# Performance work log

Hardware: AMD Instinct MI355X
Metric: run time of the kernel (lower is better)

The kernel has to match this reference:

```python
import jax, jax.numpy as jnp
import numpy as np

DIM_Q = 1024
DIM_KV = 768
N_HEADS = 4


def setup_inputs() -> dict:
    key = jax.random.key(0)
    ks = jax.random.split(key, 7)
    b, lq, lkv = 4, 2048, 2048
    q = jax.random.normal(ks[0], (b, lq, DIM_Q), dtype=jnp.float32)
    kv = jax.random.normal(ks[1], (b, lkv, DIM_KV), dtype=jnp.float32)
    s_q = 1.0 / np.sqrt(DIM_Q)
    s_kv = 1.0 / np.sqrt(DIM_KV)
    Wq = jax.random.normal(ks[2], (DIM_Q, DIM_Q), dtype=jnp.float32) * s_q
    Wk = jax.random.normal(ks[3], (DIM_Q, DIM_KV), dtype=jnp.float32) * s_kv
    Wv = jax.random.normal(ks[4], (DIM_Q, DIM_KV), dtype=jnp.float32) * s_kv
    Wo = jax.random.normal(ks[5], (DIM_Q, DIM_Q), dtype=jnp.float32) * s_q
    bo = jax.random.normal(ks[6], (DIM_Q,), dtype=jnp.float32) * 0.01
    return {"q": q, "kv": kv, "Wq": Wq, "Wk": Wk, "Wv": Wv, "Wo": Wo, "bo": bo}


def _split_heads(x):
    # [b, l, d] -> [b, h, l, d/h]
    b, l, d = x.shape
    return x.reshape(b, l, N_HEADS, d // N_HEADS).transpose(0, 2, 1, 3)


def reference(q, kv, Wq, Wk, Wv, Wo, bo):
    qp = q @ Wq.T               # [b, lq, dim_q]
    kp = kv @ Wk.T              # [b, lkv, dim_q]
    vp = kv @ Wv.T              # [b, lkv, dim_q]
    qh, kh, vh = _split_heads(qp), _split_heads(kp), _split_heads(vp)
    scale = (DIM_Q // N_HEADS) ** (-0.5)
    scores = jnp.einsum('bhqd,bhkd->bhqk', qh, kh) * scale
    attn = jax.nn.softmax(scores, axis=-1)
    ctx = jnp.einsum('bhqk,bhkd->bhqd', attn, vh)  # [b, h, lq, hd]
    b, h, lq, hd = ctx.shape
    ctx = ctx.transpose(0, 2, 1, 3).reshape(b, lq, h * hd)
    return ctx @ Wo.T + bo
```

## Files before the change

### kernel.cpp

```cpp
#include <hip/hip_runtime.h>

#define DIMQ 1024
#define NH 4
#define HD 256
#define BSZ 4
#define LQ 2048
#define LKV 2048
#define KVN 2048

typedef __attribute__((ext_vector_type(8))) short bf16x8;
typedef __attribute__((ext_vector_type(4))) float f32x4;

__device__ inline unsigned short f32_to_bf16(float f) {
  union { float f; unsigned u; } v; v.f = f;
  unsigned u = v.u;
  return (unsigned short)((u + 0x7fffu + ((u >> 16) & 1u)) >> 16);
}

__device__ inline uint4 ld8cvt(const float* p, float scale) {
  const float4 a = *(const float4*)p;
  const float4 b = *(const float4*)(p + 4);
  union { unsigned short s[8]; uint4 v; } r;
  r.s[0] = f32_to_bf16(a.x * scale); r.s[1] = f32_to_bf16(a.y * scale);
  r.s[2] = f32_to_bf16(a.z * scale); r.s[3] = f32_to_bf16(a.w * scale);
  r.s[4] = f32_to_bf16(b.x * scale); r.s[5] = f32_to_bf16(b.y * scale);
  r.s[6] = f32_to_bf16(b.z * scale); r.s[7] = f32_to_bf16(b.w * scale);
  return r.v;
}

__device__ __forceinline__ void gl2lds16(const void* gptr, void* lptr) {
  __builtin_amdgcn_global_load_lds(
      (const __attribute__((address_space(1))) void*)gptr,
      (__attribute__((address_space(3))) void*)lptr, 16, 0, 0);
}

__global__ __launch_bounds__(256)
void cvt6(const float* s0, const float* s1, const float* s2, const float* s3,
          const float* s4, const float* s5,
          unsigned short* d0, unsigned short* d1, unsigned short* d2,
          unsigned short* d3, unsigned short* d4, unsigned short* d5,
          long n0, long n1, long n2, long n3, long n4, long n5,
          float c0, float c1, float c2, float c3, float c4, float c5) {
  const float* s; unsigned short* d; long n; float c;
  switch (blockIdx.y) {
    case 0: s = s0; d = d0; n = n0; c = c0; break;
    case 1: s = s1; d = d1; n = n1; c = c1; break;
    case 2: s = s2; d = d2; n = n2; c = c2; break;
    case 3: s = s3; d = d3; n = n3; c = c3; break;
    case 4: s = s4; d = d4; n = n4; c = c4; break;
    default: s = s5; d = d5; n = n5; c = c5; break;
  }
  long i = ((long)blockIdx.x * 256 + threadIdx.x) * 8;
  if (i < n) *(uint4*)(d + i) = ld8cvt(s + i, c);
}

__global__ __launch_bounds__(256)
void transpose_k(const unsigned short* __restrict__ vp,
                 unsigned short* __restrict__ vpT,
                 int src_stride, int src_off) {
  __shared__ unsigned short T[64][64];
  const int l0g = blockIdx.x * 64;
  const int b = l0g / LKV, l0 = l0g % LKV;
  const int n0 = blockIdx.y * 64;
  const int tid = threadIdx.x;
  const int r = tid >> 3, c = tid & 7;
#pragma unroll
  for (int p = 0; p < 2; ++p) {
    int row = p * 32 + r;
    *(uint4*)&T[row][(c ^ ((row >> 3) & 7)) * 8] =
        *(const uint4*)(vp + (size_t)(l0g + row) * src_stride + src_off + n0 + c * 8);
  }
  __syncthreads();
#pragma unroll
  for (int p = 0; p < 2; ++p) {
    int n = p * 32 + r;
    union { unsigned short s[8]; uint4 v; } t;
#pragma unroll
    for (int j = 0; j < 8; ++j) {
      int row = c * 8 + j;
      t.s[j] = T[row][(((n >> 3) ^ ((row >> 3) & 7)) << 3) | (n & 7)];
    }
    *(uint4*)(vpT + ((size_t)b * DIMQ + n0 + n) * LKV + l0 + c * 8) = t.v;
  }
}

template<typename TOUT, bool HAS_BIAS>
__global__ __launch_bounds__(256)
void gemm_bt(const unsigned short* __restrict__ A,
             const unsigned short* __restrict__ Bm,
             const float* __restrict__ bias,
             TOUT* __restrict__ C,
             int M, int N, int K) {
  __shared__ alignas(16) unsigned short As[128 * 64];
  __shared__ alignas(16) unsigned short Bs[128 * 64];
  const int tid = threadIdx.x;
  const int lane = tid & 63;
  const int wave = tid >> 6;
  const int wr = (wave >> 1) * 64, wc = (wave & 1) * 64;
  const int l15 = lane & 15, quad = lane >> 4;
  const int srow = lane >> 3, scol = lane & 7;
  const int m0 = blockIdx.x * 128;
  const int n0 = blockIdx.y * 128;

  f32x4 acc[4][4] = {};
  for (int k0 = 0; k0 < K; k0 += 64) {
    __syncthreads();
#pragma unroll
    for (int i = 0; i < 4; ++i) {
      int c = wave * 4 + i;
      gl2lds16(A + (size_t)(m0 + c * 8 + srow) * K + k0 + scol * 8, As + c * 512);
      gl2lds16(Bm + (size_t)(n0 + c * 8 + srow) * K + k0 + scol * 8, Bs + c * 512);
    }
    __syncthreads();
#pragma unroll
    for (int kh = 0; kh < 2; ++kh) {
      bf16x8 af[4], bfr[4];
#pragma unroll
      for (int i = 0; i < 4; ++i)
        af[i] = *(const bf16x8*)(As + (wr + i * 16 + l15) * 64 + kh * 32 + quad * 8);
#pragma unroll
      for (int j = 0; j < 4; ++j)
        bfr[j] = *(const bf16x8*)(Bs + (wc + j * 16 + l15) * 64 + kh * 32 + quad * 8);
#pragma unroll
      for (int i = 0; i < 4; ++i)
#pragma unroll
        for (int j = 0; j < 4; ++j)
          acc[i][j] = __builtin_amdgcn_mfma_f32_16x16x32_bf16(af[i], bfr[j], acc[i][j], 0, 0, 0);
    }
  }

#pragma unroll
  for (int j = 0; j < 4; ++j) {
    int n = n0 + wc + j * 16 + l15;
    float bv = 0.f;
    if (HAS_BIAS) bv = bias[n];
#pragma unroll
    for (int i = 0; i < 4; ++i) {
      int mb = m0 + wr + i * 16 + quad * 4;
#pragma unroll
      for (int r = 0; r < 4; ++r) {
        float v = acc[i][j][r] + bv;
        if constexpr (sizeof(TOUT) == 2)
          C[(size_t)(mb + r) * N + n] = f32_to_bf16(v);
        else
          C[(size_t)(mb + r) * N + n] = v;
      }
    }
  }
}

__global__ __launch_bounds__(256, 2)
void attn(const unsigned short* __restrict__ qp,
          const unsigned short* __restrict__ kpv,
          const unsigned short* __restrict__ vpT,
          unsigned short* __restrict__ ctx) {
  __shared__ alignas(16) unsigned short Ks[64 * 256];
  __shared__ alignas(16) unsigned short Vt[256 * 64];
  __shared__ alignas(16) unsigned short Ps[64 * 64];
  __shared__ float Ls[64][2];
  const int tid = threadIdx.x, lane = tid & 63, wave = tid >> 6;
  const int l15 = lane & 15, quad = lane >> 4;
  const int qh = wave >> 1;
  const int kvh = wave & 1;
  const int lin = blockIdx.x;
  const int work = ((lin & 7) << 6) + (lin >> 3);
  const int b = work >> 7, h = (work >> 5) & 3;
  const int q0 = (work & 31) * 64;
  const size_t base = (size_t)b * LQ * DIMQ + h * HD;

  bf16x8 qf[2][8];
#pragma unroll
  for (int im = 0; im < 2; ++im) {
    const unsigned short* qrow =
        qp + base + (size_t)(q0 + qh * 32 + im * 16 + l15) * DIMQ;
#pragma unroll
    for (int s = 0; s < 8; ++s)
      qf[im][s] = *(const bf16x8*)(qrow + s * 32 + quad * 8);
  }

  f32x4 oacc[4][4] = {};
  float lrow[2][4] = {};

  const unsigned short* kb = kpv + (size_t)b * LKV * KVN + h * HD;
  const unsigned short* vtb = vpT + ((size_t)b * DIMQ + h * HD) * LKV;

  const int krow_l = lane >> 5;
  const int kcol_l = lane & 31;
  const int vrow_l = lane >> 3;
  const int vcol_l = lane & 7;

#pragma unroll
  for (int i = 0; i < 8; ++i) {
    int c = i * 4 + wave;
    int row = 2 * c + krow_l;
    int lr = (row & 32) + ((row & 15) << 1) + ((row >> 4) & 1);
    gl2lds16(kb + (size_t)lr * KVN + ((kcol_l ^ (row & 7)) << 3), Ks + c * 512);
  }
  __syncthreads();

  for (int kv0 = 0; kv0 < LKV; kv0 += 64) {
#pragma unroll
    for (int i = 0; i < 8; ++i) {
      int c = i * 4 + wave;
      int row = 8 * c + vrow_l;
      gl2lds16(vtb + (size_t)row * LKV + kv0 + ((vcol_l ^ (row & 7)) << 3),
               Vt + c * 512);
    }

    f32x4 sacc[2][2] = {};
    const int r0 = kvh * 32 + l15, r1 = r0 + 16;
    __builtin_amdgcn_s_setprio(1);
#pragma unroll
    for (int s = 0; s < 8; ++s) {
      bf16x8 kf0 = *(const bf16x8*)(Ks + r0 * 256 + (((s * 4 + quad) ^ (r0 & 7)) << 3));
      bf16x8 kf1 = *(const bf16x8*)(Ks + r1 * 256 + (((s * 4 + quad) ^ (r1 & 7)) << 3));
      sacc[0][0] = __builtin_amdgcn_mfma_f32_16x16x32_bf16(qf[0][s], kf0, sacc[0][0], 0, 0, 0);
      sacc[0][1] = __builtin_amdgcn_mfma_f32_16x16x32_bf16(qf[0][s], kf1, sacc[0][1], 0, 0, 0);
      sacc[1][0] = __builtin_amdgcn_mfma_f32_16x16x32_bf16(qf[1][s], kf0, sacc[1][0], 0, 0, 0);
      sacc[1][1] = __builtin_amdgcn_mfma_f32_16x16x32_bf16(qf[1][s], kf1, sacc[1][1], 0, 0, 0);
    }
    __builtin_amdgcn_s_setprio(0);

    const int dw = kvh * 16 + l15;
    const int t16 = dw >> 2, sub = dw & 3;
#pragma unroll
    for (int im = 0; im < 2; ++im)
#pragma unroll
      for (int i = 0; i < 4; ++i) {
        int row = qh * 32 + im * 16 + quad * 4 + i;
        float p0 = exp2f(sacc[im][0][i]);
        float p1 = exp2f(sacc[im][1][i]);
        unsigned pw = (unsigned)f32_to_bf16(p0) | ((unsigned)f32_to_bf16(p1) << 16);
        *(unsigned*)(Ps + row * 64 + (((t16 ^ (row & 7)) << 3) | (sub * 2))) = pw;
        lrow[im][i] += p0 + p1;
      }
    __syncthreads();

    if (kv0 + 64 < LKV) {
#pragma unroll
      for (int i = 0; i < 8; ++i) {
        int c = i * 4 + wave;
        int row = 2 * c + krow_l;
        int lr = (row & 32) + ((row & 15) << 1) + ((row >> 4) & 1);
        gl2lds16(kb + (size_t)(kv0 + 64 + lr) * KVN + ((kcol_l ^ (row & 7)) << 3),
                 Ks + c * 512);
      }
    }

    __builtin_amdgcn_s_setprio(1);
#pragma unroll
    for (int u = 0; u < 2; ++u) {
      bf16x8 pf[4], vf[4];
#pragma unroll
      for (int mt = 0; mt < 4; ++mt) {
        int pr = mt * 16 + l15;
        pf[mt] = *(const bf16x8*)(Ps + pr * 64 + (((u * 4 + quad) ^ (pr & 7)) << 3));
      }
#pragma unroll
      for (int nt = 0; nt < 4; ++nt) {
        int vr = wave * 64 + nt * 16 + l15;
        vf[nt] = *(const bf16x8*)(Vt + vr * 64 + (((u * 4 + quad) ^ (vr & 7)) << 3));
      }
#pragma unroll
      for (int mt = 0; mt < 4; ++mt)
#pragma unroll
        for (int nt = 0; nt < 4; ++nt)
          oacc[mt][nt] = __builtin_amdgcn_mfma_f32_16x16x32_bf16(pf[mt], vf[nt], oacc[mt][nt], 0, 0, 0);
    }
    __builtin_amdgcn_s_setprio(0);
    __syncthreads();
  }

#pragma unroll
  for (int im = 0; im < 2; ++im)
#pragma unroll
    for (int i = 0; i < 4; ++i) {
      float l = lrow[im][i];
      l += __shfl_xor(l, 1);
      l += __shfl_xor(l, 2);
      l += __shfl_xor(l, 4);
      l += __shfl_xor(l, 8);
      if (l15 == 0) Ls[qh * 32 + im * 16 + quad * 4 + i][kvh] = l;
    }
  __syncthreads();

  unsigned short* cb = ctx + base;
#pragma unroll
  for (int mt = 0; mt < 4; ++mt)
#pragma unroll
    for (int r = 0; r < 4; ++r) {
      int row = mt * 16 + quad * 4 + r;
      float inv = 1.0f / (Ls[row][0] + Ls[row][1]);
#pragma unroll
      for (int nt = 0; nt < 4; ++nt) {
        int col = wave * 64 + nt * 16 + l15;
        cb[(size_t)(q0 + row) * DIMQ + col] = f32_to_bf16(oacc[mt][nt][r] * inv);
      }
    }
}

extern "C" void kernel_launch(void* const* d_in, const int* in_sizes, int n_in,
                              void* d_out, int out_size, void* d_ws, size_t ws_size,
                              hipStream_t stream) {
  const float* q  = (const float*)d_in[0];
  const float* kv = (const float*)d_in[1];
  const float* Wq = (const float*)d_in[2];
  const float* Wk = (const float*)d_in[3];
  const float* Wv = (const float*)d_in[4];
  const float* Wo = (const float*)d_in[5];
  const float* bo = (const float*)d_in[6];
  float* out = (float*)d_out;

  const long NQ = (long)BSZ * LQ * DIMQ;
  const long NKV = (long)BSZ * LKV * 768;
  const long NWQ = (long)DIMQ * DIMQ;
  const long NWK = (long)DIMQ * 768;

  unsigned short* q_bf = (unsigned short*)d_out;
  unsigned short* kpv  = (unsigned short*)d_out;
  unsigned short* kv_bf = (unsigned short*)d_ws;
  unsigned short* ctx   = kv_bf;
  unsigned short* Wq_bf = kv_bf + NQ;
  unsigned short* Wk_bf = Wq_bf + NWQ;
  unsigned short* Wv_bf = Wk_bf + NWK;
  unsigned short* Wo_bf = Wv_bf + NWK;
  unsigned short* qp    = Wo_bf + NWQ;
  unsigned short* vpT   = qp + NQ;

  dim3 blk(256);
  const int M = BSZ * LQ;

  cvt6<<<dim3(4096, 6), blk, 0, stream>>>(
      kv, Wq, Wk, Wv, Wo, q,
      kv_bf, Wq_bf, Wk_bf, Wv_bf, Wo_bf, q_bf,
      NKV, NWQ, NWK, NWK, NWQ, NQ,
      1.0f, 0.0625f * 1.44269504088896f, 1.0f, 1.0f, 1.0f, 1.0f);
  gemm_bt<unsigned short, false><<<dim3(M/128, DIMQ/128), blk, 0, stream>>>(q_bf, Wq_bf, nullptr, qp, M, DIMQ, 1024);
  gemm_bt<unsigned short, false><<<dim3(M/128, KVN/128), blk, 0, stream>>>(kv_bf, Wk_bf, nullptr, kpv, M, KVN, 768);
  transpose_k<<<dim3(M/64, DIMQ/64), blk, 0, stream>>>(kpv, vpT, KVN, 1024);
  attn<<<dim3(512), blk, 0, stream>>>(qp, kpv, vpT, ctx);
  gemm_bt<float, true><<<dim3(M/128, DIMQ/128), blk, 0, stream>>>(ctx, Wo_bf, bo, out, M, DIMQ, 1024);
}
```

Before: 302.5 us.

## Double-buffer K/V tiles and use 512-thread blocks over 128 query rows

```diff
diff --git a/kernel.cpp b/kernel.cpp
--- a/kernel.cpp
+++ b/kernel.cpp
@@ -149,30 +149,32 @@
   }
 }
 
-__global__ __launch_bounds__(256, 2)
+__global__ __launch_bounds__(512, 1)
 void attn(const unsigned short* __restrict__ qp,
           const unsigned short* __restrict__ kpv,
           const unsigned short* __restrict__ vpT,
           unsigned short* __restrict__ ctx) {
-  __shared__ alignas(16) unsigned short Ks[64 * 256];
-  __shared__ alignas(16) unsigned short Vt[256 * 64];
-  __shared__ alignas(16) unsigned short Ps[64 * 64];
-  __shared__ float Ls[64][2];
+  __shared__ alignas(16) unsigned short Ks[2][64 * 256];
+  __shared__ alignas(16) unsigned short Vt[2][256 * 64];
+  __shared__ alignas(16) unsigned short Ps[128 * 64];
+  __shared__ float Ls[128][2];
   const int tid = threadIdx.x, lane = tid & 63, wave = tid >> 6;
   const int l15 = lane & 15, quad = lane >> 4;
-  const int qh = wave >> 1;
+  const int qqh = wave >> 1;
   const int kvh = wave & 1;
+  const int qh2 = wave >> 2;
+  const int dq  = wave & 3;
   const int lin = blockIdx.x;
-  const int work = ((lin & 7) << 6) + (lin >> 3);
-  const int b = work >> 7, h = (work >> 5) & 3;
-  const int q0 = (work & 31) * 64;
+  const int work = ((lin & 7) << 5) + (lin >> 3);
+  const int b = work >> 6, h = (work >> 4) & 3;
+  const int q0 = (work & 15) * 128;
   const size_t base = (size_t)b * LQ * DIMQ + h * HD;
 
   bf16x8 qf[2][8];
 #pragma unroll
   for (int im = 0; im < 2; ++im) {
     const unsigned short* qrow =
-        qp + base + (size_t)(q0 + qh * 32 + im * 16 + l15) * DIMQ;
+        qp + base + (size_t)(q0 + qqh * 32 + im * 16 + l15) * DIMQ;
 #pragma unroll
     for (int s = 0; s < 8; ++s)
       qf[im][s] = *(const bf16x8*)(qrow + s * 32 + quad * 8);
@@ -189,22 +191,38 @@
   const int vrow_l = lane >> 3;
   const int vcol_l = lane & 7;
 
-#pragma unroll
-  for (int i = 0; i < 8; ++i) {
-    int c = i * 4 + wave;
-    int row = 2 * c + krow_l;
-    int lr = (row & 32) + ((row & 15) << 1) + ((row >> 4) & 1);
-    gl2lds16(kb + (size_t)lr * KVN + ((kcol_l ^ (row & 7)) << 3), Ks + c * 512);
-  }
+  auto stageK = [&](int kvbase, unsigned short* dst) {
+#pragma unroll
+    for (int i = 0; i < 4; ++i) {
+      int c = i * 8 + wave;
+      int row = 2 * c + krow_l;
+      int lr = (row & 32) + ((row & 15) << 1) + ((row >> 4) & 1);
+      gl2lds16(kb + (size_t)(kvbase + lr) * KVN + ((kcol_l ^ (row & 7)) << 3),
+               dst + c * 512);
+    }
+  };
+  auto stageV = [&](int kvbase, unsigned short* dst) {
+#pragma unroll
+    for (int i = 0; i < 4; ++i) {
+      int c = i * 8 + wave;
+      int row = 8 * c + vrow_l;
+      gl2lds16(vtb + (size_t)row * LKV + kvbase + ((vcol_l ^ (row & 7)) << 3),
+               dst + c * 512);
+    }
+  };
+
+  stageK(0, Ks[0]);
+  stageV(0, Vt[0]);
   __syncthreads();
 
-  for (int kv0 = 0; kv0 < LKV; kv0 += 64) {
-#pragma unroll
-    for (int i = 0; i < 8; ++i) {
-      int c = i * 4 + wave;
-      int row = 8 * c + vrow_l;
-      gl2lds16(vtb + (size_t)row * LKV + kv0 + ((vcol_l ^ (row & 7)) << 3),
-               Vt + c * 512);
+  for (int t = 0; t < 32; ++t) {
+    const int cur = t & 1;
+    const unsigned short* KsC = Ks[cur];
+    const unsigned short* VtC = Vt[cur];
+
+    if (t < 31) {
+      stageK((t + 1) * 64, Ks[cur ^ 1]);
+      stageV((t + 1) * 64, Vt[cur ^ 1]);
     }
 
     f32x4 sacc[2][2] = {};
@@ -212,8 +230,8 @@
     __builtin_amdgcn_s_setprio(1);
 #pragma unroll
     for (int s = 0; s < 8; ++s) {
-      bf16x8 kf0 = *(const bf16x8*)(Ks + r0 * 256 + (((s * 4 + quad) ^ (r0 & 7)) << 3));
-      bf16x8 kf1 = *(const bf16x8*)(Ks + r1 * 256 + (((s * 4 + quad) ^ (r1 & 7)) << 3));
+      bf16x8 kf0 = *(const bf16x8*)(KsC + r0 * 256 + (((s * 4 + quad) ^ (r0 & 7)) << 3));
+      bf16x8 kf1 = *(const bf16x8*)(KsC + r1 * 256 + (((s * 4 + quad) ^ (r1 & 7)) << 3));
       sacc[0][0] = __builtin_amdgcn_mfma_f32_16x16x32_bf16(qf[0][s], kf0, sacc[0][0], 0, 0, 0);
       sacc[0][1] = __builtin_amdgcn_mfma_f32_16x16x32_bf16(qf[0][s], kf1, sacc[0][1], 0, 0, 0);
       sacc[1][0] = __builtin_amdgcn_mfma_f32_16x16x32_bf16(qf[1][s], kf0, sacc[1][0], 0, 0, 0);
@@ -227,25 +245,15 @@
     for (int im = 0; im < 2; ++im)
 #pragma unroll
       for (int i = 0; i < 4; ++i) {
-        int row = qh * 32 + im * 16 + quad * 4 + i;
+        int row = qqh * 32 + im * 16 + quad * 4 + i;
         float p0 = exp2f(sacc[im][0][i]);
         float p1 = exp2f(sacc[im][1][i]);
         unsigned pw = (unsigned)f32_to_bf16(p0) | ((unsigned)f32_to_bf16(p1) << 16);
         *(unsigned*)(Ps + row * 64 + (((t16 ^ (row & 7)) << 3) | (sub * 2))) = pw;
         lrow[im][i] += p0 + p1;
       }
+
     __syncthreads();
-
-    if (kv0 + 64 < LKV) {
-#pragma unroll
-      for (int i = 0; i < 8; ++i) {
-        int c = i * 4 + wave;
-        int row = 2 * c + krow_l;
-        int lr = (row & 32) + ((row & 15) << 1) + ((row >> 4) & 1);
-        gl2lds16(kb + (size_t)(kv0 + 64 + lr) * KVN + ((kcol_l ^ (row & 7)) << 3),
-                 Ks + c * 512);
-      }
-    }
 
     __builtin_amdgcn_s_setprio(1);
 #pragma unroll
@@ -253,13 +261,13 @@
       bf16x8 pf[4], vf[4];
 #pragma unroll
       for (int mt = 0; mt < 4; ++mt) {
-        int pr = mt * 16 + l15;
+        int pr = qh2 * 64 + mt * 16 + l15;
         pf[mt] = *(const bf16x8*)(Ps + pr * 64 + (((u * 4 + quad) ^ (pr & 7)) << 3));
       }
 #pragma unroll
       for (int nt = 0; nt < 4; ++nt) {
-        int vr = wave * 64 + nt * 16 + l15;
-        vf[nt] = *(const bf16x8*)(Vt + vr * 64 + (((u * 4 + quad) ^ (vr & 7)) << 3));
+        int vr = dq * 64 + nt * 16 + l15;
+        vf[nt] = *(const bf16x8*)(VtC + vr * 64 + (((u * 4 + quad) ^ (vr & 7)) << 3));
       }
 #pragma unroll
       for (int mt = 0; mt < 4; ++mt)
@@ -268,6 +276,7 @@
           oacc[mt][nt] = __builtin_amdgcn_mfma_f32_16x16x32_bf16(pf[mt], vf[nt], oacc[mt][nt], 0, 0, 0);
     }
     __builtin_amdgcn_s_setprio(0);
+
     __syncthreads();
   }
 
@@ -280,7 +289,7 @@
       l += __shfl_xor(l, 2);
       l += __shfl_xor(l, 4);
       l += __shfl_xor(l, 8);
-      if (l15 == 0) Ls[qh * 32 + im * 16 + quad * 4 + i][kvh] = l;
+      if (l15 == 0) Ls[qqh * 32 + im * 16 + quad * 4 + i][kvh] = l;
     }
   __syncthreads();
 
@@ -289,11 +298,11 @@
   for (int mt = 0; mt < 4; ++mt)
 #pragma unroll
     for (int r = 0; r < 4; ++r) {
-      int row = mt * 16 + quad * 4 + r;
+      int row = qh2 * 64 + mt * 16 + quad * 4 + r;
       float inv = 1.0f / (Ls[row][0] + Ls[row][1]);
 #pragma unroll
       for (int nt = 0; nt < 4; ++nt) {
-        int col = wave * 64 + nt * 16 + l15;
+        int col = dq * 64 + nt * 16 + l15;
         cb[(size_t)(q0 + row) * DIMQ + col] = f32_to_bf16(oacc[mt][nt][r] * inv);
       }
     }
@@ -338,6 +347,6 @@
   gemm_bt<unsigned short, false><<<dim3(M/128, DIMQ/128), blk, 0, stream>>>(q_bf, Wq_bf, nullptr, qp, M, DIMQ, 1024);
   gemm_bt<unsigned short, false><<<dim3(M/128, KVN/128), blk, 0, stream>>>(kv_bf, Wk_bf, nullptr, kpv, M, KVN, 768);
   transpose_k<<<dim3(M/64, DIMQ/64), blk, 0, stream>>>(kpv, vpT, KVN, 1024);
-  attn<<<dim3(512), blk, 0, stream>>>(qp, kpv, vpT, ctx);
+  attn<<<dim3(256), dim3(512), 0, stream>>>(qp, kpv, vpT, ctx);
   gemm_bt<float, true><<<dim3(M/128, DIMQ/128), blk, 0, stream>>>(ctx, Wo_bf, bo, out, M, DIMQ, 1024);
 }
```

New measurement: 311.3 us. +2.9%, slower.
